# Kernel optimization log

Measured on AMD Instinct MI355X. Metric: run time of the kernel, lower is better.

Reference implementation:

```python
import jax, jax.numpy as jnp
import numpy as np

B, C_FEATS, T = 8, 256, 1024
NUM_COMP = 64
EPS = 1e-9


def setup_inputs() -> dict:
    key = jax.random.key(0)
    k1, k2 = jax.random.split(key)
    x = jax.random.normal(k1, (B, C_FEATS, T), dtype=jnp.float32)
    mu = jax.random.normal(k2, (NUM_COMP, C_FEATS), dtype=jnp.float32)
    prec = jnp.ones((NUM_COMP,), dtype=jnp.float32)
    return {"x": x, "mu": mu, "prec": prec}


def reference(x, mu, prec):
    # x: (B, F, T) -> (B, T, F), matching torch transpose(1, -1)
    xt = jnp.swapaxes(x, 1, 2)
    # squared distance to each centroid via expansion (avoids (B,T,C,F) delta):
    x2 = jnp.sum(xt * xt, axis=-1, keepdims=True)            # (B, T, 1)
    mu2 = jnp.sum(mu * mu, axis=-1)                           # (C,)
    xmu = jnp.einsum('btf,cf->btc', xt, mu)                   # (B, T, C)
    dist = x2 - 2.0 * xmu + mu2                               # (B, T, C)
    llk = -(prec * prec) * dist                               # use_bias=False
    r = jax.nn.softmax(llk, axis=-1)                          # (B, T, C)
    Nraw = jnp.sum(r, axis=1)                                 # (B, C)
    N = Nraw + EPS
    # F = sum_t r*(x - mu) = sum_t r*x - (sum_t r)*mu
    F = jnp.einsum('btc,btf->bcf', r, xt) - Nraw[..., None] * mu  # (B, C, F)
    pool = F / N[..., None]
    return pool.reshape(x.shape[0], -1)                       # (B, C*F)
```

## Files before the change

kernel.cpp:

```cpp
#include <hip/hip_runtime.h>

#define BB 8
#define FF 256
#define TT 1024
#define CC 64
constexpr float EPS = 1e-9f;

#define BCF (BB * CC * FF)

#define WS_NP 0
#define WS_R  32768
#define WS_FP 557056

__global__ __launch_bounds__(256, 2) void k_phase1(
        const float* __restrict__ x, const float* __restrict__ mu,
        const float* __restrict__ prec, float* __restrict__ ws) {
    __shared__ __align__(16) float xt[16][260];
    __shared__ __align__(16) float Sred[4][16][68];
    __shared__ __align__(16) float rl[16][68];
    __shared__ float x2s[16];
    __shared__ float mu2s[CC], p2s[CC];

    const int tid = threadIdx.x;
    const int b    = blockIdx.x >> 6;
    const int tile = blockIdx.x & 63;
    const int t0   = tile * 16;
    const float* xb = x + (size_t)b * FF * TT;

    {
        const int c = tid >> 2, q = tid & 3;
        const float* mp = mu + c * FF + q * 64;
        float s = 0.f;
        #pragma unroll
        for (int i = 0; i < 16; ++i) {
            float4 v = *(const float4*)(mp + i * 4);
            s += v.x * v.x + v.y * v.y + v.z * v.z + v.w * v.w;
        }
        s += __shfl_xor(s, 1);
        s += __shfl_xor(s, 2);
        if (q == 0) mu2s[c] = s;
        if (tid < CC) { float p = prec[tid]; p2s[tid] = p * p; }
    }

    #pragma unroll
    for (int it = 0; it < 4; ++it) {
        const int id = it * 256 + tid;
        const int f = id >> 2, seg = id & 3;
        float4 v = *(const float4*)(xb + f * TT + t0 + seg * 4);
        xt[seg * 4 + 0][f] = v.x;
        xt[seg * 4 + 1][f] = v.y;
        xt[seg * 4 + 2][f] = v.z;
        xt[seg * 4 + 3][f] = v.w;
    }
    __syncthreads();

    {
        const int t = tid >> 4, kk = tid & 15;
        float s = 0.f;
        #pragma unroll
        for (int q = 0; q < 16; ++q) { float v = xt[t][kk + 16 * q]; s += v * v; }
        s += __shfl_xor(s, 1);
        s += __shfl_xor(s, 2);
        s += __shfl_xor(s, 4);
        s += __shfl_xor(s, 8);
        if (kk == 0) x2s[t] = s;
    }
    __syncthreads();

    {
        const int g = tid >> 6, lane = tid & 63;
        const int tr = lane & 7;
        const int c0 = (lane >> 3) * 8;
        float acc[2][8];
        #pragma unroll
        for (int i = 0; i < 2; ++i)
            #pragma unroll
            for (int j = 0; j < 8; ++j) acc[i][j] = 0.f;

        const float* mupt = mu + (size_t)c0 * FF + g * 64;
        #pragma unroll 4
        for (int kk = 0; kk < 16; ++kk) {
            const int f4 = g * 64 + kk * 4;
            float4 xv0 = *(const float4*)&xt[tr][f4];
            float4 xv1 = *(const float4*)&xt[tr + 8][f4];
            #pragma unroll
            for (int j = 0; j < 8; ++j) {
                float4 mv = *(const float4*)(mupt + j * FF + kk * 4);
                acc[0][j] += xv0.x * mv.x + xv0.y * mv.y + xv0.z * mv.z + xv0.w * mv.w;
                acc[1][j] += xv1.x * mv.x + xv1.y * mv.y + xv1.z * mv.z + xv1.w * mv.w;
            }
        }
        #pragma unroll
        for (int i = 0; i < 2; ++i) {
            *(float4*)&Sred[g][tr + 8 * i][c0] =
                make_float4(acc[i][0], acc[i][1], acc[i][2], acc[i][3]);
            *(float4*)&Sred[g][tr + 8 * i][c0 + 4] =
                make_float4(acc[i][4], acc[i][5], acc[i][6], acc[i][7]);
        }
    }
    __syncthreads();

    {
        const int t = tid >> 4, kk = tid & 15;
        const int c4 = kk * 4;
        float Sx = 0.f, Sy = 0.f, Sz = 0.f, Sw = 0.f;
        #pragma unroll
        for (int gg = 0; gg < 4; ++gg) {
            float4 v = *(const float4*)&Sred[gg][t][c4];
            Sx += v.x; Sy += v.y; Sz += v.z; Sw += v.w;
        }
        const float x2v = x2s[t];
        float l0 = -p2s[c4 + 0] * (x2v - 2.f * Sx + mu2s[c4 + 0]);
        float l1 = -p2s[c4 + 1] * (x2v - 2.f * Sy + mu2s[c4 + 1]);
        float l2 = -p2s[c4 + 2] * (x2v - 2.f * Sz + mu2s[c4 + 2]);
        float l3 = -p2s[c4 + 3] * (x2v - 2.f * Sw + mu2s[c4 + 3]);
        float m = fmaxf(fmaxf(l0, l1), fmaxf(l2, l3));
        m = fmaxf(m, __shfl_xor(m, 1));
        m = fmaxf(m, __shfl_xor(m, 2));
        m = fmaxf(m, __shfl_xor(m, 4));
        m = fmaxf(m, __shfl_xor(m, 8));
        float e0 = __expf(l0 - m), e1 = __expf(l1 - m);
        float e2 = __expf(l2 - m), e3 = __expf(l3 - m);
        float sum = e0 + e1 + e2 + e3;
        sum += __shfl_xor(sum, 1);
        sum += __shfl_xor(sum, 2);
        sum += __shfl_xor(sum, 4);
        sum += __shfl_xor(sum, 8);
        const float inv = 1.f / sum;
        float4 rv = make_float4(e0 * inv, e1 * inv, e2 * inv, e3 * inv);
        *(float4*)&rl[t][c4] = rv;
        const int tq = tile >> 3, tloc = (tile & 7) * 16 + t;
        *(float4*)(ws + WS_R + (((size_t)(b * 8 + tq) * 128) + tloc) * 64 + c4) = rv;
    }
    __syncthreads();

    if (tid < CC) {
        float ns = 0.f;
        #pragma unroll
        for (int t = 0; t < 16; ++t) ns += rl[t][tid];
        ws[WS_NP + (size_t)blockIdx.x * CC + tid] = ns;
    }
}

__global__ __launch_bounds__(256, 2) void k_phase2(
        const float* __restrict__ x, float* __restrict__ ws) {
    __shared__ __align__(16) float xs[64][36];
    __shared__ __align__(16) float rs[64][68];
    const int tid = threadIdx.x;
    const int bid = blockIdx.x;
    const int b = bid >> 6, fsl = (bid >> 3) & 7, tq = bid & 7;
    const int f0 = fsl * 32;
    const int t0 = tq * 128;
    const float* xb = x + (size_t)b * FF * TT;
    const float* rb = ws + WS_R + (size_t)(b * 8 + tq) * 128 * 64;

    const int fi = tid & 7, cg = tid >> 3;
    float a0[4] = {0.f, 0.f, 0.f, 0.f};
    float a1[4] = {0.f, 0.f, 0.f, 0.f};

    for (int sub = 0; sub < 2; ++sub) {
        #pragma unroll
        for (int it = 0; it < 2; ++it) {
            const int id = it * 256 + tid;
            const int ff = id >> 4, seg = id & 15;
            float4 v = *(const float4*)(xb + (f0 + ff) * TT + t0 + sub * 64 + seg * 4);
            #pragma unroll
            for (int k = 0; k < 4; ++k) {
                const int t = seg * 4 + k;
                const float e = (k == 0) ? v.x : (k == 1) ? v.y : (k == 2) ? v.z : v.w;
                xs[t][ff ^ ((t & 7) << 2)] = e;
            }
        }
        #pragma unroll
        for (int it = 0; it < 4; ++it) {
            const int id = it * 256 + tid;
            float4 v = *(const float4*)(rb + (size_t)sub * 4096 + id * 4);
            *(float4*)&rs[id >> 4][(id & 15) * 4] = v;
        }
        __syncthreads();

        #pragma unroll 8
        for (int t = 0; t < 64; ++t) {
            float4 xv = *(const float4*)&xs[t][(fi * 4) ^ ((t & 7) << 2)];
            float2 rv = *(const float2*)&rs[t][cg * 2];
            a0[0] += rv.x * xv.x; a0[1] += rv.x * xv.y;
            a0[2] += rv.x * xv.z; a0[3] += rv.x * xv.w;
            a1[0] += rv.y * xv.x; a1[1] += rv.y * xv.y;
            a1[2] += rv.y * xv.z; a1[3] += rv.y * xv.w;
        }
        __syncthreads();
    }

    float* fp = ws + WS_FP + (size_t)tq * BCF + (size_t)b * CC * FF + f0;
    *(float4*)(fp + (size_t)(cg * 2 + 0) * FF + fi * 4) =
        make_float4(a0[0], a0[1], a0[2], a0[3]);
    *(float4*)(fp + (size_t)(cg * 2 + 1) * FF + fi * 4) =
        make_float4(a1[0], a1[1], a1[2], a1[3]);
}

__global__ __launch_bounds__(256, 2) void k_phase3(
        const float* __restrict__ mu, const float* __restrict__ ws,
        float* __restrict__ out) {
    __shared__ float nsh[1];
    const int tid = threadIdx.x;
    const int b = blockIdx.x >> 6, c = blockIdx.x & 63;
    if (tid < 64) {
        float s = ws[WS_NP + (size_t)(b * 64 + tid) * CC + c];
        #pragma unroll
        for (int k = 1; k < 64; k <<= 1) s += __shfl_xor(s, k);
        if (tid == 0) nsh[0] = s;
    }
    __syncthreads();
    const float nr = nsh[0];
    const int f = tid;
    const float* fp = ws + WS_FP + ((size_t)b * CC + c) * FF + f;
    float fs = 0.f;
    #pragma unroll
    for (int p = 0; p < 8; ++p) fs += fp[(size_t)p * BCF];
    out[((size_t)b * CC + c) * FF + f] = (fs - nr * mu[c * FF + f]) / (nr + EPS);
}

extern "C" void kernel_launch(void* const* d_in, const int* in_sizes, int n_in,
                              void* d_out, int out_size, void* d_ws, size_t ws_size,
                              hipStream_t stream) {
    const float* x    = (const float*)d_in[0];
    const float* mu   = (const float*)d_in[1];
    const float* prec = (const float*)d_in[2];
    float* out = (float*)d_out;
    float* ws  = (float*)d_ws;

    k_phase1<<<512, 256, 0, stream>>>(x, mu, prec, ws);
    k_phase2<<<512, 256, 0, stream>>>(x, ws);
    k_phase3<<<512, 256, 0, stream>>>(mu, ws, out);
}
```

Measured before the change: 34.46 us.

## Double threads per block and split phase-2 time axis into sixteen partials

Phase 1 now runs 512 threads per block. It splits the feature dot-product across 8 groups instead of 4 and handles two centroids per thread in the softmax; one barrier is removed because a later barrier already orders the x2 reads. Phase 2 uses 512-thread blocks covering 64 features by 64 timesteps in a single pass, dropping the XOR swizzle and the inner two-step loop. Phase 3 then sums 16 time partials instead of 8. The aim is more parallelism and fewer barrier round-trips, at the cost of twice the partial-F workspace traffic and tighter register limits from the new launch bounds.

```diff
diff --git a/kernel.cpp b/kernel.cpp
--- a/kernel.cpp
+++ b/kernel.cpp
@@ -12,11 +12,11 @@
 #define WS_R  32768
 #define WS_FP 557056
 
-__global__ __launch_bounds__(256, 2) void k_phase1(
+__global__ __launch_bounds__(512, 4) void k_phase1(
         const float* __restrict__ x, const float* __restrict__ mu,
         const float* __restrict__ prec, float* __restrict__ ws) {
     __shared__ __align__(16) float xt[16][260];
-    __shared__ __align__(16) float Sred[4][16][68];
+    __shared__ __align__(16) float Sred[8][16][68];
     __shared__ __align__(16) float rl[16][68];
     __shared__ float x2s[16];
     __shared__ float mu2s[CC], p2s[CC];
@@ -28,23 +28,24 @@
     const float* xb = x + (size_t)b * FF * TT;
 
     {
-        const int c = tid >> 2, q = tid & 3;
-        const float* mp = mu + c * FF + q * 64;
+        const int c = tid >> 3, q = tid & 7;
+        const float* mp = mu + c * FF + q * 4;
         float s = 0.f;
         #pragma unroll
-        for (int i = 0; i < 16; ++i) {
-            float4 v = *(const float4*)(mp + i * 4);
+        for (int i = 0; i < 8; ++i) {
+            float4 v = *(const float4*)(mp + i * 32);
             s += v.x * v.x + v.y * v.y + v.z * v.z + v.w * v.w;
         }
         s += __shfl_xor(s, 1);
         s += __shfl_xor(s, 2);
+        s += __shfl_xor(s, 4);
         if (q == 0) mu2s[c] = s;
         if (tid < CC) { float p = prec[tid]; p2s[tid] = p * p; }
     }
 
     #pragma unroll
-    for (int it = 0; it < 4; ++it) {
-        const int id = it * 256 + tid;
+    for (int it = 0; it < 2; ++it) {
+        const int id = it * 512 + tid;
         const int f = id >> 2, seg = id & 3;
         float4 v = *(const float4*)(xb + f * TT + t0 + seg * 4);
         xt[seg * 4 + 0][f] = v.x;
@@ -55,17 +56,17 @@
     __syncthreads();
 
     {
-        const int t = tid >> 4, kk = tid & 15;
+        const int t = tid >> 5, kk = tid & 31;
         float s = 0.f;
         #pragma unroll
-        for (int q = 0; q < 16; ++q) { float v = xt[t][kk + 16 * q]; s += v * v; }
+        for (int q = 0; q < 8; ++q) { float v = xt[t][kk + 32 * q]; s += v * v; }
         s += __shfl_xor(s, 1);
         s += __shfl_xor(s, 2);
         s += __shfl_xor(s, 4);
         s += __shfl_xor(s, 8);
+        s += __shfl_xor(s, 16);
         if (kk == 0) x2s[t] = s;
     }
-    __syncthreads();
 
     {
         const int g = tid >> 6, lane = tid & 63;
@@ -77,10 +78,10 @@
             #pragma unroll
             for (int j = 0; j < 8; ++j) acc[i][j] = 0.f;
 
-        const float* mupt = mu + (size_t)c0 * FF + g * 64;
+        const float* mupt = mu + (size_t)c0 * FF + g * 32;
         #pragma unroll 4
-        for (int kk = 0; kk < 16; ++kk) {
-            const int f4 = g * 64 + kk * 4;
+        for (int kk = 0; kk < 8; ++kk) {
+            const int f4 = g * 32 + kk * 4;
             float4 xv0 = *(const float4*)&xt[tr][f4];
             float4 xv1 = *(const float4*)&xt[tr + 8][f4];
             #pragma unroll
@@ -101,36 +102,37 @@
     __syncthreads();
 
     {
-        const int t = tid >> 4, kk = tid & 15;
-        const int c4 = kk * 4;
-        float Sx = 0.f, Sy = 0.f, Sz = 0.f, Sw = 0.f;
-        #pragma unroll
-        for (int gg = 0; gg < 4; ++gg) {
-            float4 v = *(const float4*)&Sred[gg][t][c4];
-            Sx += v.x; Sy += v.y; Sz += v.z; Sw += v.w;
+        const int t = tid >> 5, kk = tid & 31;
+        const int c2 = kk * 2;
+        float Sx = 0.f, Sy = 0.f;
+        #pragma unroll
+        for (int gg = 0; gg < 8; ++gg) {
+            float2 v = *(const float2*)&Sred[gg][t][c2];
+            Sx += v.x; Sy += v.y;
         }
         const float x2v = x2s[t];
-        float l0 = -p2s[c4 + 0] * (x2v - 2.f * Sx + mu2s[c4 + 0]);
-        float l1 = -p2s[c4 + 1] * (x2v - 2.f * Sy + mu2s[c4 + 1]);
-        float l2 = -p2s[c4 + 2] * (x2v - 2.f * Sz + mu2s[c4 + 2]);
-        float l3 = -p2s[c4 + 3] * (x2v - 2.f * Sw + mu2s[c4 + 3]);
-        float m = fmaxf(fmaxf(l0, l1), fmaxf(l2, l3));
+        float l0 = -p2s[c2 + 0] * (x2v - 2.f * Sx + mu2s[c2 + 0]);
+        float l1 = -p2s[c2 + 1] * (x2v - 2.f * Sy + mu2s[c2 + 1]);
+        float m = fmaxf(l0, l1);
         m = fmaxf(m, __shfl_xor(m, 1));
         m = fmaxf(m, __shfl_xor(m, 2));
         m = fmaxf(m, __shfl_xor(m, 4));
         m = fmaxf(m, __shfl_xor(m, 8));
+        m = fmaxf(m, __shfl_xor(m, 16));
         float e0 = __expf(l0 - m), e1 = __expf(l1 - m);
-        float e2 = __expf(l2 - m), e3 = __expf(l3 - m);
-        float sum = e0 + e1 + e2 + e3;
+        float sum = e0 + e1;
         sum += __shfl_xor(sum, 1);
         sum += __shfl_xor(sum, 2);
         sum += __shfl_xor(sum, 4);
         sum += __shfl_xor(sum, 8);
+        sum += __shfl_xor(sum, 16);
         const float inv = 1.f / sum;
-        float4 rv = make_float4(e0 * inv, e1 * inv, e2 * inv, e3 * inv);
-        *(float4*)&rl[t][c4] = rv;
-        const int tq = tile >> 3, tloc = (tile & 7) * 16 + t;
-        *(float4*)(ws + WS_R + (((size_t)(b * 8 + tq) * 128) + tloc) * 64 + c4) = rv;
+        const float r0 = e0 * inv, r1 = e1 * inv;
+        rl[t][c2] = r0;
+        rl[t][c2 + 1] = r1;
+        const int tq = tile >> 2, tloc = (tile & 3) * 16 + t;
+        *(float2*)(ws + WS_R + (((size_t)(b * 16 + tq) * 64) + tloc) * 64 + c2) =
+            make_float2(r0, r1);
     }
     __syncthreads();
 
@@ -142,53 +144,49 @@
     }
 }
 
-__global__ __launch_bounds__(256, 2) void k_phase2(
+__global__ __launch_bounds__(512, 4) void k_phase2(
         const float* __restrict__ x, float* __restrict__ ws) {
-    __shared__ __align__(16) float xs[64][36];
+    __shared__ __align__(16) float xs[64][68];
     __shared__ __align__(16) float rs[64][68];
     const int tid = threadIdx.x;
     const int bid = blockIdx.x;
-    const int b = bid >> 6, fsl = (bid >> 3) & 7, tq = bid & 7;
-    const int f0 = fsl * 32;
-    const int t0 = tq * 128;
+    const int b   = bid >> 6;
+    const int fsl = (bid >> 4) & 3;
+    const int tq  = bid & 15;
+    const int f0  = fsl * 64;
+    const int t0  = tq * 64;
     const float* xb = x + (size_t)b * FF * TT;
-    const float* rb = ws + WS_R + (size_t)(b * 8 + tq) * 128 * 64;
-
-    const int fi = tid & 7, cg = tid >> 3;
+    const float* rb = ws + WS_R + (size_t)(b * 16 + tq) * 64 * 64;
+
+    #pragma unroll
+    for (int it = 0; it < 2; ++it) {
+        const int id = it * 512 + tid;
+        const int ff = id >> 4, seg = id & 15;
+        float4 v = *(const float4*)(xb + (f0 + ff) * TT + t0 + seg * 4);
+        xs[seg * 4 + 0][ff] = v.x;
+        xs[seg * 4 + 1][ff] = v.y;
+        xs[seg * 4 + 2][ff] = v.z;
+        xs[seg * 4 + 3][ff] = v.w;
+    }
+    #pragma unroll
+    for (int it = 0; it < 2; ++it) {
+        const int id = it * 512 + tid;
+        float4 v = *(const float4*)(rb + (size_t)id * 4);
+        *(float4*)&rs[id >> 4][(id & 15) * 4] = v;
+    }
+    __syncthreads();
+
+    const int fi = tid & 15, cg = tid >> 4;
     float a0[4] = {0.f, 0.f, 0.f, 0.f};
     float a1[4] = {0.f, 0.f, 0.f, 0.f};
-
-    for (int sub = 0; sub < 2; ++sub) {
-        #pragma unroll
-        for (int it = 0; it < 2; ++it) {
-            const int id = it * 256 + tid;
-            const int ff = id >> 4, seg = id & 15;
-            float4 v = *(const float4*)(xb + (f0 + ff) * TT + t0 + sub * 64 + seg * 4);
-            #pragma unroll
-            for (int k = 0; k < 4; ++k) {
-                const int t = seg * 4 + k;
-                const float e = (k == 0) ? v.x : (k == 1) ? v.y : (k == 2) ? v.z : v.w;
-                xs[t][ff ^ ((t & 7) << 2)] = e;
-            }
-        }
-        #pragma unroll
-        for (int it = 0; it < 4; ++it) {
-            const int id = it * 256 + tid;
-            float4 v = *(const float4*)(rb + (size_t)sub * 4096 + id * 4);
-            *(float4*)&rs[id >> 4][(id & 15) * 4] = v;
-        }
-        __syncthreads();
-
-        #pragma unroll 8
-        for (int t = 0; t < 64; ++t) {
-            float4 xv = *(const float4*)&xs[t][(fi * 4) ^ ((t & 7) << 2)];
-            float2 rv = *(const float2*)&rs[t][cg * 2];
-            a0[0] += rv.x * xv.x; a0[1] += rv.x * xv.y;
-            a0[2] += rv.x * xv.z; a0[3] += rv.x * xv.w;
-            a1[0] += rv.y * xv.x; a1[1] += rv.y * xv.y;
-            a1[2] += rv.y * xv.z; a1[3] += rv.y * xv.w;
-        }
-        __syncthreads();
+    #pragma unroll 8
+    for (int t = 0; t < 64; ++t) {
+        float4 xv = *(const float4*)&xs[t][fi * 4];
+        float2 rv = *(const float2*)&rs[t][cg * 2];
+        a0[0] += rv.x * xv.x; a0[1] += rv.x * xv.y;
+        a0[2] += rv.x * xv.z; a0[3] += rv.x * xv.w;
+        a1[0] += rv.y * xv.x; a1[1] += rv.y * xv.y;
+        a1[2] += rv.y * xv.z; a1[3] += rv.y * xv.w;
     }
 
     float* fp = ws + WS_FP + (size_t)tq * BCF + (size_t)b * CC * FF + f0;
@@ -198,7 +196,7 @@
         make_float4(a1[0], a1[1], a1[2], a1[3]);
 }
 
-__global__ __launch_bounds__(256, 2) void k_phase3(
+__global__ __launch_bounds__(256) void k_phase3(
         const float* __restrict__ mu, const float* __restrict__ ws,
         float* __restrict__ out) {
     __shared__ float nsh[1];
@@ -216,7 +214,7 @@
     const float* fp = ws + WS_FP + ((size_t)b * CC + c) * FF + f;
     float fs = 0.f;
     #pragma unroll
-    for (int p = 0; p < 8; ++p) fs += fp[(size_t)p * BCF];
+    for (int p = 0; p < 16; ++p) fs += fp[(size_t)p * BCF];
     out[((size_t)b * CC + c) * FF + f] = (fs - nr * mu[c * FF + f]) / (nr + EPS);
 }
 
@@ -229,7 +227,7 @@
     float* out = (float*)d_out;
     float* ws  = (float*)d_ws;
 
-    k_phase1<<<512, 256, 0, stream>>>(x, mu, prec, ws);
-    k_phase2<<<512, 256, 0, stream>>>(x, ws);
+    k_phase1<<<512, 512, 0, stream>>>(x, mu, prec, ws);
+    k_phase2<<<512, 512, 0, stream>>>(x, ws);
     k_phase3<<<512, 256, 0, stream>>>(mu, ws, out);
 }
```

Measured after the change: 44.10 us. 1.28x slower.

## Fuse r-weighted x accumulation into phase1 and drop the separate phase2 kernel

Applied to the files above, without the earlier changes.

Each phase1 block now multiplies its softmax responsibilities by its transposed x tile while both are still in shared memory. It writes a per-block 64x256 partial F to workspace. This removes the phase2 launch, the global round trip of r, and the second read of x. The cost is 64 partial sums per (b,c,f) instead of 8, so the workspace grows to about 32 MB written and then read back by phase3. The fused kernel also carries 64 accumulators per thread.

```diff
diff --git a/kernel.cpp b/kernel.cpp
--- a/kernel.cpp
+++ b/kernel.cpp
@@ -6,13 +6,10 @@
 #define CC 64
 constexpr float EPS = 1e-9f;
 
-#define BCF (BB * CC * FF)
-
 #define WS_NP 0
-#define WS_R  32768
-#define WS_FP 557056
-
-__global__ __launch_bounds__(256, 2) void k_phase1(
+#define WS_FP 32768
+
+__global__ __launch_bounds__(256, 2) void k_fused(
         const float* __restrict__ x, const float* __restrict__ mu,
         const float* __restrict__ prec, float* __restrict__ ws) {
     __shared__ __align__(16) float xt[16][260];
@@ -127,10 +124,7 @@
         sum += __shfl_xor(sum, 4);
         sum += __shfl_xor(sum, 8);
         const float inv = 1.f / sum;
-        float4 rv = make_float4(e0 * inv, e1 * inv, e2 * inv, e3 * inv);
-        *(float4*)&rl[t][c4] = rv;
-        const int tq = tile >> 3, tloc = (tile & 7) * 16 + t;
-        *(float4*)(ws + WS_R + (((size_t)(b * 8 + tq) * 128) + tloc) * 64 + c4) = rv;
+        *(float4*)&rl[t][c4] = make_float4(e0 * inv, e1 * inv, e2 * inv, e3 * inv);
     }
     __syncthreads();
 
@@ -140,62 +134,42 @@
         for (int t = 0; t < 16; ++t) ns += rl[t][tid];
         ws[WS_NP + (size_t)blockIdx.x * CC + tid] = ns;
     }
-}
-
-__global__ __launch_bounds__(256, 2) void k_phase2(
-        const float* __restrict__ x, float* __restrict__ ws) {
-    __shared__ __align__(16) float xs[64][36];
-    __shared__ __align__(16) float rs[64][68];
-    const int tid = threadIdx.x;
-    const int bid = blockIdx.x;
-    const int b = bid >> 6, fsl = (bid >> 3) & 7, tq = bid & 7;
-    const int f0 = fsl * 32;
-    const int t0 = tq * 128;
-    const float* xb = x + (size_t)b * FF * TT;
-    const float* rb = ws + WS_R + (size_t)(b * 8 + tq) * 128 * 64;
-
-    const int fi = tid & 7, cg = tid >> 3;
-    float a0[4] = {0.f, 0.f, 0.f, 0.f};
-    float a1[4] = {0.f, 0.f, 0.f, 0.f};
-
-    for (int sub = 0; sub < 2; ++sub) {
-        #pragma unroll
-        for (int it = 0; it < 2; ++it) {
-            const int id = it * 256 + tid;
-            const int ff = id >> 4, seg = id & 15;
-            float4 v = *(const float4*)(xb + (f0 + ff) * TT + t0 + sub * 64 + seg * 4);
-            #pragma unroll
-            for (int k = 0; k < 4; ++k) {
-                const int t = seg * 4 + k;
-                const float e = (k == 0) ? v.x : (k == 1) ? v.y : (k == 2) ? v.z : v.w;
-                xs[t][ff ^ ((t & 7) << 2)] = e;
+
+    {
+        const int fc = tid & 15;
+        const int c0 = (tid >> 4) * 4;
+        float a2[4][4][4];
+        #pragma unroll
+        for (int j = 0; j < 4; ++j)
+            #pragma unroll
+            for (int q = 0; q < 4; ++q)
+                #pragma unroll
+                for (int e = 0; e < 4; ++e) a2[j][q][e] = 0.f;
+
+        #pragma unroll 4
+        for (int t = 0; t < 16; ++t) {
+            float4 rv = *(const float4*)&rl[t][c0];
+            #pragma unroll
+            for (int q = 0; q < 4; ++q) {
+                float4 xv = *(const float4*)&xt[t][fc * 4 + 64 * q];
+                a2[0][q][0] += rv.x * xv.x; a2[0][q][1] += rv.x * xv.y;
+                a2[0][q][2] += rv.x * xv.z; a2[0][q][3] += rv.x * xv.w;
+                a2[1][q][0] += rv.y * xv.x; a2[1][q][1] += rv.y * xv.y;
+                a2[1][q][2] += rv.y * xv.z; a2[1][q][3] += rv.y * xv.w;
+                a2[2][q][0] += rv.z * xv.x; a2[2][q][1] += rv.z * xv.y;
+                a2[2][q][2] += rv.z * xv.z; a2[2][q][3] += rv.z * xv.w;
+                a2[3][q][0] += rv.w * xv.x; a2[3][q][1] += rv.w * xv.y;
+                a2[3][q][2] += rv.w * xv.z; a2[3][q][3] += rv.w * xv.w;
             }
         }
-        #pragma unroll
-        for (int it = 0; it < 4; ++it) {
-            const int id = it * 256 + tid;
-            float4 v = *(const float4*)(rb + (size_t)sub * 4096 + id * 4);
-            *(float4*)&rs[id >> 4][(id & 15) * 4] = v;
-        }
-        __syncthreads();
-
-        #pragma unroll 8
-        for (int t = 0; t < 64; ++t) {
-            float4 xv = *(const float4*)&xs[t][(fi * 4) ^ ((t & 7) << 2)];
-            float2 rv = *(const float2*)&rs[t][cg * 2];
-            a0[0] += rv.x * xv.x; a0[1] += rv.x * xv.y;
-            a0[2] += rv.x * xv.z; a0[3] += rv.x * xv.w;
-            a1[0] += rv.y * xv.x; a1[1] += rv.y * xv.y;
-            a1[2] += rv.y * xv.z; a1[3] += rv.y * xv.w;
-        }
-        __syncthreads();
-    }
-
-    float* fp = ws + WS_FP + (size_t)tq * BCF + (size_t)b * CC * FF + f0;
-    *(float4*)(fp + (size_t)(cg * 2 + 0) * FF + fi * 4) =
-        make_float4(a0[0], a0[1], a0[2], a0[3]);
-    *(float4*)(fp + (size_t)(cg * 2 + 1) * FF + fi * 4) =
-        make_float4(a1[0], a1[1], a1[2], a1[3]);
+        float* fp = ws + WS_FP + (size_t)blockIdx.x * CC * FF;
+        #pragma unroll
+        for (int j = 0; j < 4; ++j)
+            #pragma unroll
+            for (int q = 0; q < 4; ++q)
+                *(float4*)(fp + (size_t)(c0 + j) * FF + fc * 4 + 64 * q) =
+                    make_float4(a2[j][q][0], a2[j][q][1], a2[j][q][2], a2[j][q][3]);
+    }
 }
 
 __global__ __launch_bounds__(256, 2) void k_phase3(
@@ -213,10 +187,10 @@
     __syncthreads();
     const float nr = nsh[0];
     const int f = tid;
-    const float* fp = ws + WS_FP + ((size_t)b * CC + c) * FF + f;
+    const float* fp = ws + WS_FP + ((size_t)(b * 64) * CC + c) * FF + f;
     float fs = 0.f;
-    #pragma unroll
-    for (int p = 0; p < 8; ++p) fs += fp[(size_t)p * BCF];
+    #pragma unroll 8
+    for (int p = 0; p < 64; ++p) fs += fp[(size_t)p * CC * FF];
     out[((size_t)b * CC + c) * FF + f] = (fs - nr * mu[c * FF + f]) / (nr + EPS);
 }
 
@@ -229,7 +203,6 @@
     float* out = (float*)d_out;
     float* ws  = (float*)d_ws;
 
-    k_phase1<<<512, 256, 0, stream>>>(x, mu, prec, ws);
-    k_phase2<<<512, 256, 0, stream>>>(x, ws);
+    k_fused<<<512, 256, 0, stream>>>(x, mu, prec, ws);
     k_phase3<<<512, 256, 0, stream>>>(mu, ws, out);
 }
```

New measurement: 38.90 us. +12.9%, slower.
